# Kernel tuning notes

Hardware: AMD Instinct MI355X
Metric: run time of the kernel (lower is better)

The kernel has to match this reference:

```python
import jax, jax.numpy as jnp
import numpy as np

B, C_IN, C_OUT, K, H, W = 32, 128, 256, 3, 56, 56
STRIDE, PAD = 1, 1


def setup_inputs() -> dict:
    key = jax.random.key(0)
    kx, kw, kb = jax.random.split(key, 3)
    x = jax.random.normal(kx, (B, C_IN, H, W), dtype=jnp.float32)
    weight = jax.random.normal(kw, (C_OUT, C_IN, K, K), dtype=jnp.float32)
    bias = jax.random.normal(kb, (C_OUT,), dtype=jnp.float32)
    return {"x": x, "weight": weight, "bias": bias}


def reference(x, weight, bias):
    # Binarize weights to {-1, 0, +1} exactly like torch.sign
    w_bin = jnp.sign(weight)
    out = jax.lax.conv_general_dilated(
        x, w_bin,
        window_strides=(STRIDE, STRIDE),
        padding=[(PAD, PAD), (PAD, PAD)],
        dimension_numbers=("NCHW", "OIHW", "NCHW"),
    )
    return out + bias[None, :, None, None]
```

## Files before the change

### kernel.cpp

```cpp
#include <hip/hip_runtime.h>
#include <cstdint>
#include <cstddef>

typedef _Float16 f16;
typedef _Float16 f16x4 __attribute__((ext_vector_type(4)));
typedef _Float16 f16x8 __attribute__((ext_vector_type(8)));
typedef float    f32x4 __attribute__((ext_vector_type(4)));

#define CIN    128
#define COUT   256
#define HH     56
#define WW     56
#define HW     3136
#define PPDIM  3364
#define XPLANE (PPDIM*CIN)

__device__ __forceinline__ void gload16(const void* g, void* l) {
  __builtin_amdgcn_global_load_lds((const __attribute__((address_space(1))) unsigned int*)g,
                                   (__attribute__((address_space(3))) unsigned int*)l,
                                   16, 0, 0);
}

__global__ __launch_bounds__(256) void xpad_kernel(const float* __restrict__ x,
                                                   f16* __restrict__ xp) {
  const int bid = blockIdx.x;
  const int pr  = bid % 58;
  const int b   = bid / 58;
  const int tid = threadIdx.x;
  f16* orow = xp + (size_t)b * XPLANE + (size_t)pr * 58 * CIN;

  if (pr == 0 || pr == 57) {
    for (int i = tid; i < 928; i += 256)
      *(f16x8*)(orow + (size_t)i * 8) = (f16x8){};
    return;
  }
  const int h = pr - 1;
  const int wave = tid >> 6, lane = tid & 63;
  if (tid < 32) {
    int px = (tid < 16) ? 0 : 57;
    int cg = tid & 15;
    *(f16x8*)(orow + (size_t)px * CIN + cg * 8) = (f16x8){};
  }
  if (lane < 56) {
    const float* xb = x + (size_t)b * CIN * HW + (size_t)h * WW + lane;
    f16* op = orow + (size_t)(lane + 1) * CIN;
    #pragma unroll
    for (int cg = 0; cg < 4; ++cg) {
      const int c0 = (wave * 4 + cg) * 8;
      f16x8 v;
      #pragma unroll
      for (int j = 0; j < 8; ++j)
        v[j] = (f16)xb[(size_t)(c0 + j) * HW];
      *(f16x8*)(op + c0) = v;
    }
  }
}

__global__ __launch_bounds__(256) void wprep_kernel(const float* __restrict__ w,
                                                    f16* __restrict__ wt) {
  int t = blockIdx.x * 256 + threadIdx.x;
  int s     = t >> 14;
  int hidx  = t & 16383;
  int co    = hidx >> 6;
  int khalf = (hidx & 63) ^ ((co & 7) << 3);
  int kidx  = s >> 1;
  int c     = ((s & 1) << 6) + khalf;
  float v = w[(size_t)co * 1152 + c * 9 + kidx];
  wt[t] = (f16)((v > 0.f) ? 1.f : (v < 0.f ? -1.f : 0.f));
}

__global__ __launch_bounds__(512) void bconv_main(
    const f16* __restrict__ xp, const f16* __restrict__ wt,
    const float* __restrict__ bias, float* __restrict__ out) {
  __shared__ __align__(16) f16 Alds[128 * 64];
  __shared__ __align__(16) f16 Blds[256 * 64];
  const int tid = threadIdx.x;
  const int p0  = blockIdx.x * 128;

  const int wave = tid >> 6, lane = tid & 63;
  const int pxl  = tid >> 3;
  const int kx_s = ((tid & 7) << 4) ^ ((pxl & 7) << 4);
  const int pga  = p0 + pxl;
  const int pgb  = pga + 64;
  const int ba = pga / HW, ra = pga % HW;
  const int bb = pgb / HW, rb = pgb % HW;
  const int ha = ra / WW, wa = ra % WW;
  const int hb = rb / WW, wb = rb % WW;
  const char* xpB = (const char*)xp;
  const char* srcA0 = xpB + 2 * ((size_t)ba * XPLANE + (size_t)((ha + 1) * 58 + wa + 1) * CIN) + kx_s;
  const char* srcA1 = xpB + 2 * ((size_t)bb * XPLANE + (size_t)((hb + 1) * 58 + wb + 1) * CIN) + kx_s;
  char* AldsB = (char*)Alds;
  char* BldsB = (char*)Blds;
  char* dstA0 = AldsB + (wave << 10);
  char* dstA1 = AldsB + 8192 + (wave << 10);
  const char* wtB = (const char*)wt + (tid << 4);
  char* dstB = BldsB + (wave << 10);

  const int wpx = wave >> 2;
  const int wco = wave & 3;
  const int l15 = lane & 15, l4 = lane >> 4;
  const int kxr = (l15 & 7) << 4;
  const int rA = ((wpx << 6) + l15) << 7;
  const int rB = ((wco << 6) + l15) << 7;

  f32x4 acc[4][4];
  #pragma unroll
  for (int i = 0; i < 4; ++i)
    #pragma unroll
    for (int j = 0; j < 4; ++j) acc[i][j] = (f32x4){0.f, 0.f, 0.f, 0.f};

  #pragma unroll 1
  for (int s = 0; s < 18; ++s) {
    const int kidx = s >> 1, ch = s & 1;
    const int dh = kidx / 3 - 1, dw = kidx - (kidx / 3) * 3 - 1;
    const long toff = (long)(dh * 58 + dw) * 256 + ch * 128;
    gload16(srcA0 + toff, dstA0);
    gload16(srcA1 + toff, dstA1);
    const char* ws = wtB + (size_t)s * 32768;
    gload16(ws,         dstB);
    gload16(ws + 8192,  dstB + 8192);
    gload16(ws + 16384, dstB + 16384);
    gload16(ws + 24576, dstB + 24576);
    __syncthreads();

    #pragma unroll
    for (int kk = 0; kk < 2; ++kk) {
      const int ko = ((kk << 6) + (l4 << 4)) ^ kxr;
      f16x8 xf[4], wf[4];
      #pragma unroll
      for (int j = 0; j < 4; ++j)
        xf[j] = *(const f16x8*)(AldsB + rA + (j << 11) + ko);
      #pragma unroll
      for (int i = 0; i < 4; ++i)
        wf[i] = *(const f16x8*)(BldsB + rB + (i << 11) + ko);
      #pragma unroll
      for (int i = 0; i < 4; ++i)
        #pragma unroll
        for (int j = 0; j < 4; ++j)
          acc[i][j] = __builtin_amdgcn_mfma_f32_16x16x32_f16(wf[i], xf[j], acc[i][j], 0, 0, 0);
    }
    __syncthreads();
  }

  #pragma unroll
  for (int j = 0; j < 4; ++j) {
    const int pg = p0 + wpx * 64 + j * 16 + l15;
    const int bo = pg / HW;
    const int pr = pg % HW;
    float* ob = out + (size_t)bo * (COUT * HW) + pr;
    #pragma unroll
    for (int i = 0; i < 4; ++i) {
      const int cb2 = wco * 64 + i * 16 + l4 * 4;
      #pragma unroll
      for (int r = 0; r < 4; ++r) {
        const int co = cb2 + r;
        ob[(size_t)co * HW] = acc[i][j][r] + bias[co];
      }
    }
  }
}

extern "C" void kernel_launch(void* const* d_in, const int* in_sizes, int n_in,
                              void* d_out, int out_size, void* d_ws, size_t ws_size,
                              hipStream_t stream) {
  const float* x    = (const float*)d_in[0];
  const float* w    = (const float*)d_in[1];
  const float* bias = (const float*)d_in[2];
  float* out = (float*)d_out;

  f16* xp = (f16*)d_ws;
  f16* wt = xp + (size_t)32 * XPLANE;

  xpad_kernel<<<1856, 256, 0, stream>>>(x, xp);
  wprep_kernel<<<1152, 256, 0, stream>>>(w, wt);
  bconv_main<<<784, 512, 0, stream>>>(xp, wt, bias, out);
}
```

Measured before the change: 210.3 us.

## Double-buffer activation tiles, load weights directly to registers, swizzle block order

The main conv kernel now uses 256 threads with four waves, each covering 64 pixels by 128 output channels (32 accumulators). Activation tiles are double-buffered in LDS so the next tap's 64-channel half is prefetched while the current one is computed. Weights bypass LDS and are read straight from global memory into registers, using an unswizzled layout. Block indices are remapped for cache locality and MFMA sections run at raised wave priority. The larger per-wave accumulator tile raises register pressure and can limit occupancy.

```diff
diff --git a/kernel.cpp b/kernel.cpp
--- a/kernel.cpp
+++ b/kernel.cpp
@@ -59,103 +59,112 @@
 __global__ __launch_bounds__(256) void wprep_kernel(const float* __restrict__ w,
                                                     f16* __restrict__ wt) {
   int t = blockIdx.x * 256 + threadIdx.x;
-  int s     = t >> 14;
-  int hidx  = t & 16383;
-  int co    = hidx >> 6;
-  int khalf = (hidx & 63) ^ ((co & 7) << 3);
-  int kidx  = s >> 1;
-  int c     = ((s & 1) << 6) + khalf;
+  int s    = t >> 14;
+  int hidx = t & 16383;
+  int co   = hidx >> 6;
+  int kl   = hidx & 63;
+  int kidx = s >> 1;
+  int c    = ((s & 1) << 6) + kl;
   float v = w[(size_t)co * 1152 + c * 9 + kidx];
   wt[t] = (f16)((v > 0.f) ? 1.f : (v < 0.f ? -1.f : 0.f));
 }
 
-__global__ __launch_bounds__(512) void bconv_main(
+__global__ __launch_bounds__(256, 2) void bconv_main(
     const f16* __restrict__ xp, const f16* __restrict__ wt,
     const float* __restrict__ bias, float* __restrict__ out) {
-  __shared__ __align__(16) f16 Alds[128 * 64];
-  __shared__ __align__(16) f16 Blds[256 * 64];
+  __shared__ __align__(16) f16 Alds[16384];
   const int tid = threadIdx.x;
-  const int p0  = blockIdx.x * 128;
+  const int bid = blockIdx.x;
+  const int swz = (bid & 7) * 98 + (bid >> 3);
+  const int p0  = swz * 128;
+
+  const int rl   = tid >> 3;
+  const int kx_s = ((tid & 7) << 4) ^ ((rl & 7) << 4);
+  const char* srcA[4];
+  #pragma unroll
+  for (int q = 0; q < 4; ++q) {
+    int pg = p0 + q * 32 + rl;
+    int b = pg / HW, r = pg % HW;
+    int h = r / WW,  w = r % WW;
+    srcA[q] = (const char*)xp +
+              2 * ((size_t)b * XPLANE + (size_t)((h + 1) * 58 + (w + 1)) * CIN) + kx_s;
+  }
+  char* AldsB = (char*)Alds;
+  const int dst_t = tid << 4;
 
   const int wave = tid >> 6, lane = tid & 63;
-  const int pxl  = tid >> 3;
-  const int kx_s = ((tid & 7) << 4) ^ ((pxl & 7) << 4);
-  const int pga  = p0 + pxl;
-  const int pgb  = pga + 64;
-  const int ba = pga / HW, ra = pga % HW;
-  const int bb = pgb / HW, rb = pgb % HW;
-  const int ha = ra / WW, wa = ra % WW;
-  const int hb = rb / WW, wb = rb % WW;
-  const char* xpB = (const char*)xp;
-  const char* srcA0 = xpB + 2 * ((size_t)ba * XPLANE + (size_t)((ha + 1) * 58 + wa + 1) * CIN) + kx_s;
-  const char* srcA1 = xpB + 2 * ((size_t)bb * XPLANE + (size_t)((hb + 1) * 58 + wb + 1) * CIN) + kx_s;
-  char* AldsB = (char*)Alds;
-  char* BldsB = (char*)Blds;
-  char* dstA0 = AldsB + (wave << 10);
-  char* dstA1 = AldsB + 8192 + (wave << 10);
-  const char* wtB = (const char*)wt + (tid << 4);
-  char* dstB = BldsB + (wave << 10);
+  const int wm = wave >> 1;
+  const int wn = wave & 1;
+  const int l15 = lane & 15, l4 = lane >> 4;
+  const int off0 = (l4 << 4) ^ ((l15 & 7) << 4);
+  const int off1 = (64 + (l4 << 4)) ^ ((l15 & 7) << 4);
+  const int xrow_base = (wm * 64 + l15) << 7;
+  const f16* wfp = wt + ((size_t)(wn * 128 + l15) << 6) + (l4 << 3);
 
-  const int wpx = wave >> 2;
-  const int wco = wave & 3;
-  const int l15 = lane & 15, l4 = lane >> 4;
-  const int kxr = (l15 & 7) << 4;
-  const int rA = ((wpx << 6) + l15) << 7;
-  const int rB = ((wco << 6) + l15) << 7;
-
-  f32x4 acc[4][4];
+  f32x4 acc[8][4];
   #pragma unroll
-  for (int i = 0; i < 4; ++i)
+  for (int i = 0; i < 8; ++i)
     #pragma unroll
     for (int j = 0; j < 4; ++j) acc[i][j] = (f32x4){0.f, 0.f, 0.f, 0.f};
 
+  #pragma unroll
+  for (int q = 0; q < 4; ++q)
+    gload16(srcA[q] - 15104, AldsB + q * 4096 + dst_t);
+  __syncthreads();
+
+  auto TILE = [&](int rb, int wb, int TT, long toff, bool dostage) {
+    f16x8 wf[8][2];
+    const f16* ws = wfp + ((size_t)TT << 14);
+    #pragma unroll
+    for (int i = 0; i < 8; ++i) {
+      wf[i][0] = *(const f16x8*)(ws + i * 1024);
+      wf[i][1] = *(const f16x8*)(ws + i * 1024 + 32);
+    }
+    #pragma unroll
+    for (int j = 0; j < 4; ++j) {
+      if (j < 2 && dostage) {
+        gload16(srcA[2 * j]     + toff, AldsB + wb + (2 * j) * 4096     + dst_t);
+        gload16(srcA[2 * j + 1] + toff, AldsB + wb + (2 * j + 1) * 4096 + dst_t);
+      }
+      const char* xrow = AldsB + rb + xrow_base + (j << 11);
+      f16x8 xf0 = *(const f16x8*)(xrow + off0);
+      f16x8 xf1 = *(const f16x8*)(xrow + off1);
+      __builtin_amdgcn_s_setprio(1);
+      #pragma unroll
+      for (int i = 0; i < 8; ++i)
+        acc[i][j] = __builtin_amdgcn_mfma_f32_16x16x32_f16(wf[i][0], xf0, acc[i][j], 0, 0, 0);
+      #pragma unroll
+      for (int i = 0; i < 8; ++i)
+        acc[i][j] = __builtin_amdgcn_mfma_f32_16x16x32_f16(wf[i][1], xf1, acc[i][j], 0, 0, 0);
+      __builtin_amdgcn_s_setprio(0);
+    }
+  };
+
   #pragma unroll 1
-  for (int s = 0; s < 18; ++s) {
-    const int kidx = s >> 1, ch = s & 1;
-    const int dh = kidx / 3 - 1, dw = kidx - (kidx / 3) * 3 - 1;
-    const long toff = (long)(dh * 58 + dw) * 256 + ch * 128;
-    gload16(srcA0 + toff, dstA0);
-    gload16(srcA1 + toff, dstA1);
-    const char* ws = wtB + (size_t)s * 32768;
-    gload16(ws,         dstB);
-    gload16(ws + 8192,  dstB + 8192);
-    gload16(ws + 16384, dstB + 16384);
-    gload16(ws + 24576, dstB + 24576);
+  for (int it = 0; it < 9; ++it) {
+    const int dh = it / 3 - 1, dw = it % 3 - 1;
+    const long toff_o = ((long)(dh * 58 + dw) * 128 + 64) * 2;
+    const int kn = (it < 8) ? (it + 1) : 8;
+    const int dh2 = kn / 3 - 1, dw2 = kn % 3 - 1;
+    const long toff_e = ((long)(dh2 * 58 + dw2) * 128) * 2;
+    TILE(0, 16384, 2 * it, toff_o, true);
     __syncthreads();
-
-    #pragma unroll
-    for (int kk = 0; kk < 2; ++kk) {
-      const int ko = ((kk << 6) + (l4 << 4)) ^ kxr;
-      f16x8 xf[4], wf[4];
-      #pragma unroll
-      for (int j = 0; j < 4; ++j)
-        xf[j] = *(const f16x8*)(AldsB + rA + (j << 11) + ko);
-      #pragma unroll
-      for (int i = 0; i < 4; ++i)
-        wf[i] = *(const f16x8*)(BldsB + rB + (i << 11) + ko);
-      #pragma unroll
-      for (int i = 0; i < 4; ++i)
-        #pragma unroll
-        for (int j = 0; j < 4; ++j)
-          acc[i][j] = __builtin_amdgcn_mfma_f32_16x16x32_f16(wf[i], xf[j], acc[i][j], 0, 0, 0);
-    }
+    TILE(16384, 0, 2 * it + 1, toff_e, it < 8);
     __syncthreads();
   }
 
   #pragma unroll
   for (int j = 0; j < 4; ++j) {
-    const int pg = p0 + wpx * 64 + j * 16 + l15;
+    const int pg = p0 + wm * 64 + j * 16 + l15;
     const int bo = pg / HW;
     const int pr = pg % HW;
     float* ob = out + (size_t)bo * (COUT * HW) + pr;
     #pragma unroll
-    for (int i = 0; i < 4; ++i) {
-      const int cb2 = wco * 64 + i * 16 + l4 * 4;
+    for (int i = 0; i < 8; ++i) {
+      const int cb = wn * 128 + i * 16 + l4 * 4;
       #pragma unroll
-      for (int r = 0; r < 4; ++r) {
-        const int co = cb2 + r;
-        ob[(size_t)co * HW] = acc[i][j][r] + bias[co];
-      }
+      for (int r = 0; r < 4; ++r)
+        ob[(size_t)(cb + r) * HW] = acc[i][j][r] + bias[cb + r];
     }
   }
 }
@@ -173,5 +182,5 @@
 
   xpad_kernel<<<1856, 256, 0, stream>>>(x, xp);
   wprep_kernel<<<1152, 256, 0, stream>>>(w, wt);
-  bconv_main<<<784, 512, 0, stream>>>(xp, wt, bias, out);
+  bconv_main<<<784, 256, 0, stream>>>(xp, wt, bias, out);
 }
```

Result: slower. 307.3 us (+46.1%).
